# Performance work log

Measured on AMD Instinct MI355X. Metric: run time of the kernel, lower is better.

Reference implementation:

```python
import jax, jax.numpy as jnp
import numpy as np

N = 16384          # nodes
E_R = 524288       # radial edges (avg degree 32)
E_B = 32768        # bonded edges
N_TYPES = 20       # atom types
CS = 64            # scalar (0e) channels
CV = 32            # vector (1o) channels
EA = 16            # edge_attr_dim
EA_B = EA // 2     # bondedness embedding dim
EA_R = (EA + 1) // 2  # radial basis dim
CUTOFF = 1.5       # effective_radial_cutoff
L = 2              # n_layers
NORM = float(np.sqrt((E_R + E_B) / N))  # ~sqrt(avg degree) message normalization


def setup_inputs() -> dict:
    key = jax.random.key(0)
    ks = jax.random.split(key, 32)
    def rn(i, shape, scale=1.0):
        return jax.random.normal(ks[i], shape, dtype=jnp.float32) * scale
    s_e = 1.0 / np.sqrt(EA)
    inp = {}
    inp["pos"] = rn(0, (N, 3))
    inp["c_noise"] = rn(1, (1,))
    inp["atom_types"] = jax.random.randint(ks[2], (N,), 0, N_TYPES)
    inp["radial_edge_index"] = jax.random.randint(ks[3], (2, E_R), 0, N)
    inp["bonded_edge_index"] = jax.random.randint(ks[4], (2, E_B), 0, N)
    # learned parameters
    inp["atom_tab"] = rn(5, (N_TYPES, CS))
    inp["bond_tab"] = rn(6, (2, EA_B))
    inp["ns0_w"] = rn(7, (CS,), 0.1)
    inp["We0"] = rn(8, (EA, CS), s_e)
    inp["We1"] = rn(9, (EA, CS), s_e)
    inp["Wself0"] = rn(10, (CS, CS), 1.0 / np.sqrt(CS))
    inp["Ws0"] = rn(11, (CS, CS), 1.0 / np.sqrt(CS))
    inp["Wv0"] = rn(12, (CS, CV), 1.0 / np.sqrt(CS))
    inp["ns_w"] = rn(13, (L, CS + CV), 0.1)
    inp["We_ss"] = rn(14, (L, EA, CS), s_e)
    inp["We_vs"] = rn(15, (L, EA, CV), s_e)
    inp["We_sv"] = rn(16, (L, EA, CS), s_e)
    inp["We_vv"] = rn(17, (L, EA, CV), s_e)
    inp["We_vx"] = rn(18, (L, EA, CV), s_e)
    inp["Wmix_s"] = rn(19, (L, CS + CV, CS), 1.0 / np.sqrt(CS + CV))
    inp["Wmix_v"] = rn(20, (L, CS + 2 * CV, CV), 1.0 / np.sqrt(CS + 2 * CV))
    inp["Wself_s"] = rn(21, (L, CS, CS), 1.0 / np.sqrt(CS))
    inp["Wself_v"] = rn(22, (L, CV, CV), 1.0 / np.sqrt(CV))
    inp["skip_w"] = rn(23, (L, 2 * (CS + CV)), 0.1)
    inp["skip_b"] = rn(24, (L, 2 * (CS + CV)), 0.1)
    inp["w_out"] = rn(25, (CV,), 1.0 / np.sqrt(CV))
    inp["gain"] = jnp.asarray(0.5, dtype=jnp.float32)
    return inp


def _radial_basis(d):
    # e3nn soft_one_hot_linspace, basis='gaussian', cutoff=True
    centers = jnp.linspace(0.0, CUTOFF, EA_R + 2)[1:-1]
    step = centers[1] - centers[0]
    diff = (d[:, None] - centers[None, :]) / step
    return jnp.exp(-diff * diff) * 1.12


def reference(pos, c_noise, atom_tab, bond_tab, ns0_w, We0, We1, Wself0, Ws0, Wv0,
              ns_w, We_ss, We_vs, We_sv, We_vv, We_vx, Wmix_s, Wmix_v, Wself_s, Wself_v,
              skip_w, skip_b, w_out, gain, atom_types, radial_edge_index, bonded_edge_index):
    edge_index = jnp.concatenate([radial_edge_index, bonded_edge_index], axis=1)
    bond_mask = jnp.concatenate([jnp.zeros((E_R,), jnp.int32), jnp.ones((E_B,), jnp.int32)])
    src, dst = edge_index[0], edge_index[1]
    edge_vec = pos[src] - pos[dst]                      # [E,3]
    d = jnp.sqrt(jnp.sum(edge_vec * edge_vec, -1) + 1e-12)
    Y1 = jnp.sqrt(3.0) * edge_vec / d[:, None]          # l=1 SH, component norm; Y0 == 1
    edge_attr = jnp.concatenate([bond_tab[bond_mask], _radial_basis(d)], axis=-1)  # [E,EA]

    # atom embedding + initial noise-conditional scaling
    s = atom_tab[atom_types] * (1.0 + c_noise * ns0_w)  # [N,CS]

    # initial projector: scalar-input equivariant conv -> hidden irreps
    w0 = edge_attr @ We0
    w1 = edge_attr @ We1
    s_src = s[src]
    a_s = jax.ops.segment_sum(w0 * s_src, dst, num_segments=N) / NORM
    a_v = jax.ops.segment_sum((w1 * s_src)[:, :, None] * Y1[:, None, :], dst, num_segments=N) / NORM
    s_h = a_s @ Ws0 + s @ Wself0                        # [N,CS]
    v_h = jnp.einsum('nci,cd->ndi', a_v, Wv0)           # [N,CV,3]

    for l in range(L):
        # noise-conditional scaling (per-irrep-channel scalar scale)
        scale = 1.0 + c_noise * ns_w[l]
        ss = s_h * scale[:CS]
        vv = v_h * scale[CS:][None, :, None]
        ss_e = ss[src]
        vv_e = vv[src]
        # edge-attr-conditioned tensor-product weights
        w_ss = edge_attr @ We_ss[l]
        w_vs = edge_attr @ We_vs[l]
        w_sv = edge_attr @ We_sv[l]
        w_vv = edge_attr @ We_vv[l]
        w_vx = edge_attr @ We_vx[l]
        # CG tensor-product messages: 0x0->0, 1x1->0 (dot), 0x1->1, 1x0->1, 1x1->1 (cross)
        vdot = jnp.einsum('eci,ei->ec', vv_e, Y1)
        m_s = jnp.concatenate([w_ss * ss_e, w_vs * vdot], axis=-1)          # [E,CS+CV]
        m_v = jnp.concatenate([
            (w_sv * ss_e)[:, :, None] * Y1[:, None, :],
            w_vv[:, :, None] * vv_e,
            w_vx[:, :, None] * jnp.cross(vv_e, Y1[:, None, :]),
        ], axis=1)                                                          # [E,CS+2CV,3]
        a_s = jax.ops.segment_sum(m_s, dst, num_segments=N) / NORM
        a_v = jax.ops.segment_sum(m_v, dst, num_segments=N) / NORM
        new_s = a_s @ Wmix_s[l] + ss @ Wself_s[l]
        new_v = jnp.einsum('nci,cd->ndi', a_v, Wmix_v[l]) + jnp.einsum('nci,cd->ndi', vv, Wself_v[l])
        # noise-conditional skip connection (gated residual)
        g = jax.nn.sigmoid(skip_b[l] + c_noise * skip_w[l])
        s_h = g[:CS] * s_h + g[CS:2 * CS] * new_s
        g_v = g[2 * CS:]
        v_h = g_v[:CV][None, :, None] * v_h + g_v[CV:][None, :, None] * new_v

    # output head: 1o vectors -> 3D displacement, times output gain
    return jnp.einsum('nci,c->ni', v_h, w_out) * gain
```

## Files before the change

### kernel.cpp

```cpp
#include <hip/hip_runtime.h>
#include <math.h>

#define NA 16384
#define ER 524288
#define EB 32768
#define ET 557056
#define INV_NORM 0.17149858514250882f
#define SQRT3 1.7320508075688772f
#define RB_STEP (1.5f/9.0f)
#define BINS 512
#define DMAX 2.5f
#define INV_H ((float)BINS / DMAX)
#define TBLU (2 * BINS * 128)

typedef unsigned int uint32;
typedef unsigned short ushort16;

__device__ __forceinline__ float sigmoidf_(float x) { return 1.f / (1.f + __expf(-x)); }

__device__ __forceinline__ ushort16 f2bf(float x) {
  uint32 u = __float_as_uint(x);
  u = u + 0x7FFFu + ((u >> 16) & 1u);
  return (ushort16)(u >> 16);
}
__device__ __forceinline__ uint32 packbf(float hi, float lo) {
  return ((uint32)f2bf(hi) << 16) | (uint32)f2bf(lo);
}
__device__ __forceinline__ float bfhi(uint32 u) { return __uint_as_float(u & 0xFFFF0000u); }
__device__ __forceinline__ float bflo(uint32 u) { return __uint_as_float(u << 16); }

__device__ __forceinline__ int edge_dst(int e, const int* __restrict__ rad, const int* __restrict__ bon) {
  return (e < ER) ? rad[ER + e] : bon[EB + (e - ER)];
}

__global__ void k_zero(int* __restrict__ count) {
  count[blockIdx.x * 256 + threadIdx.x] = 0;
}

__global__ void k_hist(const int* __restrict__ rad, const int* __restrict__ bon, int* __restrict__ count) {
  int e = blockIdx.x * 256 + threadIdx.x;
  atomicAdd(&count[edge_dst(e, rad, bon)], 1);
}

__global__ void k_scan1(const int* __restrict__ count, int* __restrict__ partial) {
  __shared__ int red[256];
  int b = blockIdx.x, t = threadIdx.x;
  red[t] = count[b * 256 + t];
  __syncthreads();
  for (int s = 128; s > 0; s >>= 1) {
    if (t < s) red[t] += red[t + s];
    __syncthreads();
  }
  if (t == 0) partial[b] = red[0];
}

__global__ void k_scan2(int* __restrict__ partial) {
  int run = 0;
  for (int i = 0; i < 64; ++i) { int c = partial[i]; partial[i] = run; run += c; }
}

__global__ void k_scan3(const int* __restrict__ count, const int* __restrict__ partial,
                        int* __restrict__ offsets, int* __restrict__ cursor) {
  __shared__ int sc[256];
  int b = blockIdx.x, t = threadIdx.x;
  int v = count[b * 256 + t];
  sc[t] = v;
  __syncthreads();
  for (int off = 1; off < 256; off <<= 1) {
    int x = (t >= off) ? sc[t - off] : 0;
    __syncthreads();
    sc[t] += x;
    __syncthreads();
  }
  int excl = sc[t] - v + partial[b];
  offsets[b * 256 + t] = excl;
  cursor[b * 256 + t] = excl;
  if (b == 63 && t == 255) offsets[NA] = excl + v;
}

__global__ void k_fill(const int* __restrict__ rad, const int* __restrict__ bon,
                       int* __restrict__ cursor, int* __restrict__ sorted) {
  int e = blockIdx.x * 256 + threadIdx.x;
  int d = edge_dst(e, rad, bon);
  int slot = atomicAdd(&cursor[d], 1);
  sorted[slot] = e;
}

__global__ void k_edge_pre(const float* __restrict__ pos,
                           const int* __restrict__ rad, const int* __restrict__ bon,
                           const int* __restrict__ sorted, float* __restrict__ rec8) {
  int idx = blockIdx.x * 256 + threadIdx.x;
  int e = sorted[idx];
  int src, dst, v;
  if (e < ER) { src = rad[e]; dst = rad[ER + e]; v = 0; }
  else        { src = bon[e - ER]; dst = bon[EB + e - ER]; v = 1; }
  float dx = pos[src * 3] - pos[dst * 3];
  float dy = pos[src * 3 + 1] - pos[dst * 3 + 1];
  float dz = pos[src * 3 + 2] - pos[dst * 3 + 2];
  float dist = sqrtf(dx * dx + dy * dy + dz * dz + 1e-12f);
  float inv = 1.f / dist;
  float fq = fminf(dist * INV_H, BINS - 1.001f);
  int q = (int)fq;
  float frac = fq - (float)q;
  int qoff = (v * BINS + q) << 7;
  float* rp = rec8 + (size_t)idx * 8;
  *(float4*)rp = make_float4(__int_as_float(src), SQRT3 * dx * inv, SQRT3 * dy * inv, SQRT3 * dz * inv);
  rp[4] = frac;
  rp[5] = __int_as_float(qoff);
}

__global__ void k_build(const float* __restrict__ We0, const float* __restrict__ We1,
                        const float* __restrict__ We_ss, const float* __restrict__ We_vs,
                        const float* __restrict__ We_sv, const float* __restrict__ We_vv,
                        const float* __restrict__ We_vx, const float* __restrict__ bond_tab,
                        uint32* __restrict__ tabs) {
  int q = blockIdx.x, t = blockIdx.y, v = blockIdx.z, c = threadIdx.x;
  float d0 = q * (DMAX / BINS), d1 = (q + 1) * (DMAX / BINS);
  float rb0[8], rb1[8];
#pragma unroll
  for (int k = 0; k < 8; ++k) {
    float f0 = (d0 - (k + 1) * RB_STEP) * (1.f / RB_STEP);
    float f1 = (d1 - (k + 1) * RB_STEP) * (1.f / RB_STEP);
    rb0[k] = 1.12f * __expf(-f0 * f0);
    rb1[k] = 1.12f * __expf(-f1 * f1);
  }
  const float* A;
  const float* B;
  int stride, coff;
  bool hasB = true;
  if (t == 0) { A = We0; B = We1; stride = 64; coff = c; }
  else if (t == 1 || t == 3) {
    int l = (t == 3);
    A = We_ss + l * 1024; B = We_sv + l * 1024; stride = 64; coff = c;
  } else {
    int l = (t == 4);
    stride = 32; coff = c & 31;
    if (c < 32) { A = We_vs + l * 512; B = We_vv + l * 512; }
    else        { A = We_vx + l * 512; B = nullptr; hasB = false; }
  }
  float ba = 0, bb = 0, a0 = 0, a1 = 0, b0 = 0, b1 = 0;
#pragma unroll
  for (int k = 0; k < 8; ++k) {
    float bt = bond_tab[v * 8 + k];
    float av_lo = A[k * stride + coff], av_hi = A[(8 + k) * stride + coff];
    ba += bt * av_lo;
    a0 += rb0[k] * av_hi; a1 += rb1[k] * av_hi;
    if (hasB) {
      float bv_lo = B[k * stride + coff], bv_hi = B[(8 + k) * stride + coff];
      bb += bt * bv_lo;
      b0 += rb0[k] * bv_hi; b1 += rb1[k] * bv_hi;
    }
  }
  uint32* o = tabs + (size_t)t * TBLU + (((size_t)v * BINS + q) << 7) + c * 2;
  o[0] = packbf(ba + a0, a1 - a0);
  o[1] = hasB ? packbf(bb + b0, b1 - b0) : 0u;
}

__global__ void k_embed(const float* __restrict__ atom_tab, const int* __restrict__ types,
                        const float* __restrict__ ns0_w, const float* __restrict__ cnoise,
                        float* __restrict__ s_feat, ushort16* __restrict__ s_bf) {
  int tid = blockIdx.x * 256 + threadIdx.x;
  int n = tid >> 6, c = tid & 63;
  float cn = cnoise[0];
  float v = atom_tab[types[n] * 64 + c] * (1.f + cn * ns0_w[c]);
  s_feat[tid] = v;
  s_bf[tid] = f2bf(v);
}

__global__ __launch_bounds__(256, 6) void k_agg0(
    const int* __restrict__ offsets, const float* __restrict__ rec8,
    const uint32* __restrict__ T0, const ushort16* __restrict__ s_bf,
    float* __restrict__ a_s, float* __restrict__ a_v) {
  int lane = threadIdx.x & 63;
  int n = blockIdx.x * 4 + (threadIdx.x >> 6);
  float acc = 0, a0 = 0, a1 = 0, a2 = 0;
  int beg = __builtin_amdgcn_readfirstlane(offsets[n]);
  int end = __builtin_amdgcn_readfirstlane(offsets[n + 1]);
  if (beg < end) {
    const float* rp0 = rec8 + (size_t)beg * 8;
    float4 rA = *(const float4*)rp0;
    float2 rB = *(const float2*)(rp0 + 4);
    int i1 = beg + (beg + 1 < end ? 1 : 0);
    const float* rp1 = rec8 + (size_t)i1 * 8;
    float4 nA = *(const float4*)rp1;
    float2 nB = *(const float2*)(rp1 + 4);
    uint2 t2 = *(const uint2*)(T0 + __float_as_int(rB.y) + (lane << 1));
    ushort16 su = s_bf[((size_t)__float_as_int(rA.x) << 6) + lane];
#pragma unroll 2
    for (int idx = beg; idx < end; ++idx) {
      uint2 pt2 = *(const uint2*)(T0 + __float_as_int(nB.y) + (lane << 1));
      ushort16 psu = s_bf[((size_t)__float_as_int(nA.x) << 6) + lane];
      int i2 = (idx + 2 < end) ? idx + 2 : end - 1;
      const float* rp2 = rec8 + (size_t)i2 * 8;
      float4 fA = *(const float4*)rp2;
      float2 fB = *(const float2*)(rp2 + 4);
      float frac = rB.x;
      float w0 = fmaf(frac, bflo(t2.x), bfhi(t2.x));
      float w1 = fmaf(frac, bflo(t2.y), bfhi(t2.y));
      float sv = __uint_as_float((uint32)su << 16);
      acc += w0 * sv;
      float t = w1 * sv;
      a0 += t * rA.y; a1 += t * rA.z; a2 += t * rA.w;
      rA = nA; rB = nB; nA = fA; nB = fB; t2 = pt2; su = psu;
    }
  }
  a_s[n * 64 + lane] = acc * INV_NORM;
  *(float4*)(a_v + ((size_t)n << 8) + (lane << 2)) =
      make_float4(a0 * INV_NORM, a1 * INV_NORM, a2 * INV_NORM, 0.f);
}

__global__ __launch_bounds__(256, 6) void k_agg_layer(
    const float* __restrict__ cnoise, const float* __restrict__ nsw,
    const int* __restrict__ offsets, const float* __restrict__ rec8,
    const uint32* __restrict__ TS, const uint32* __restrict__ TU,
    const ushort16* __restrict__ sh_bf, const uint32* __restrict__ vh_bf,
    float* __restrict__ a_s, float* __restrict__ a_v) {
  int lane = threadIdx.x & 63;
  int n = blockIdx.x * 4 + (threadIdx.x >> 6);
  int vc = lane & 31;
  bool low = lane < 32;
  float cn = cnoise[0];
  float scale_s = 1.f + cn * nsw[lane];
  float scale_v = 1.f + cn * nsw[64 + vc];

  float ms = 0;
  float av0 = 0, av1 = 0, av2 = 0;
  float ms2 = 0;
  float b0 = 0, b1 = 0, b2 = 0;
  int beg = __builtin_amdgcn_readfirstlane(offsets[n]);
  int end = __builtin_amdgcn_readfirstlane(offsets[n + 1]);
  if (beg < end) {
    const float* rp0 = rec8 + (size_t)beg * 8;
    float4 rA = *(const float4*)rp0;
    float2 rB = *(const float2*)(rp0 + 4);
    int i1 = beg + (beg + 1 < end ? 1 : 0);
    const float* rp1 = rec8 + (size_t)i1 * 8;
    float4 nA = *(const float4*)rp1;
    float2 nB = *(const float2*)(rp1 + 4);
    int src0 = __float_as_int(rA.x);
    int qo0 = __float_as_int(rB.y);
    uint2 tS = *(const uint2*)(TS + qo0 + (lane << 1));
    uint2 tU = *(const uint2*)(TU + qo0 + (lane << 1));
    ushort16 su = sh_bf[((size_t)src0 << 6) + lane];
    uint2 vv = *(const uint2*)(vh_bf + ((size_t)src0 << 6) + (vc << 1));
#pragma unroll 2
    for (int idx = beg; idx < end; ++idx) {
      int nsrc = __float_as_int(nA.x);
      int nqo = __float_as_int(nB.y);
      uint2 ptS = *(const uint2*)(TS + nqo + (lane << 1));
      uint2 ptU = *(const uint2*)(TU + nqo + (lane << 1));
      ushort16 psu = sh_bf[((size_t)nsrc << 6) + lane];
      uint2 pvv = *(const uint2*)(vh_bf + ((size_t)nsrc << 6) + (vc << 1));
      int i2 = (idx + 2 < end) ? idx + 2 : end - 1;
      const float* rp2 = rec8 + (size_t)i2 * 8;
      float4 fA = *(const float4*)rp2;
      float2 fB = *(const float2*)(rp2 + 4);
      float frac = rB.x;
      float y0 = rA.y, y1 = rA.z, y2 = rA.w;
      float wS  = fmaf(frac, bflo(tS.x), bfhi(tS.x));
      float wSV = fmaf(frac, bflo(tS.y), bfhi(tS.y));
      float wA  = fmaf(frac, bflo(tU.x), bfhi(tU.x));
      float wB  = fmaf(frac, bflo(tU.y), bfhi(tU.y));
      float ss = __uint_as_float((uint32)su << 16);
      float v0 = bfhi(vv.x), v1 = bflo(vv.x), v2 = bfhi(vv.y);
      ms += wS * ss;
      float t = wSV * ss;
      av0 += t * y0; av1 += t * y1; av2 += t * y2;
      float vdot = v0 * y0 + v1 * y1 + v2 * y2;
      ms2 += wA * vdot;
      float cx = v1 * y2 - v2 * y1;
      float cy = v2 * y0 - v0 * y2;
      float cz = v0 * y1 - v1 * y0;
      float m0 = low ? v0 : cx;
      float m1 = low ? v1 : cy;
      float m2 = low ? v2 : cz;
      float wM = low ? wB : wA;
      b0 += wM * m0; b1 += wM * m1; b2 += wM * m2;
      rA = nA; rB = nB; nA = fA; nB = fB;
      tS = ptS; tU = ptU; su = psu; vv = pvv;
    }
  }
  float fs = scale_s * INV_NORM;
  float fv = scale_v * INV_NORM;
  a_s[n * 96 + lane] = ms * fs;
  float* avn = a_v + ((size_t)n << 9);
  *(float4*)(avn + (lane << 2)) = make_float4(av0 * fs, av1 * fs, av2 * fs, 0.f);
  if (low) {
    a_s[n * 96 + 64 + vc] = ms2 * fv;
    *(float4*)(avn + ((64 + vc) << 2)) = make_float4(b0 * fv, b1 * fv, b2 * fv, 0.f);
  } else {
    *(float4*)(avn + ((96 + vc) << 2)) = make_float4(b0 * fv, b1 * fv, b2 * fv, 0.f);
  }
}

__global__ __launch_bounds__(256, 4) void k_init_s(
    const float* __restrict__ a_s, const float* __restrict__ s_feat,
    const float* __restrict__ Ws0, const float* __restrict__ Wself0,
    float* __restrict__ sh, ushort16* __restrict__ sh_bf) {
  __shared__ float W1[64 * 64];
  __shared__ float W2[64 * 64];
  __shared__ float La[8 * 64];
  __shared__ float Lf[8 * 64];
  int tid = threadIdx.x;
  for (int i = tid; i < 1024; i += 256) {
    ((float4*)W1)[i] = ((const float4*)Ws0)[i];
    ((float4*)W2)[i] = ((const float4*)Wself0)[i];
  }
  int base = blockIdx.x * 8;
  for (int i = tid; i < 512; i += 256) {
    La[i] = a_s[(size_t)base * 64 + i];
    Lf[i] = s_feat[(size_t)base * 64 + i];
  }
  __syncthreads();
  int d = tid & 63, g = tid >> 6;
  int n0 = base + g * 2;
  const float* A0 = La + g * 128;
  const float* A1 = A0 + 64;
  const float* F0 = Lf + g * 128;
  const float* F1 = F0 + 64;
  float a0 = 0, a1 = 0;
#pragma unroll 8
  for (int c = 0; c < 64; ++c) {
    float w1 = W1[c * 64 + d], w2 = W2[c * 64 + d];
    a0 += A0[c] * w1 + F0[c] * w2;
    a1 += A1[c] * w1 + F1[c] * w2;
  }
  sh[(size_t)n0 * 64 + d] = a0;
  sh[(size_t)(n0 + 1) * 64 + d] = a1;
  sh_bf[(size_t)n0 * 64 + d] = f2bf(a0);
  sh_bf[(size_t)(n0 + 1) * 64 + d] = f2bf(a1);
}

__global__ __launch_bounds__(256, 4) void k_init_v(
    const float* __restrict__ a_v, const float* __restrict__ Wv0,
    float* __restrict__ vh, uint32* __restrict__ vh_bf) {
  __shared__ float W[64 * 32];
  int tid = threadIdx.x;
  for (int i = tid; i < 512; i += 256) ((float4*)W)[i] = ((const float4*)Wv0)[i];
  __syncthreads();
  int d = tid & 31, g = tid >> 5;
  int n = blockIdx.x * 8 + g;
  const float4* av = (const float4*)(a_v + ((size_t)n << 8));
  float x = 0, y = 0, z = 0;
#pragma unroll 4
  for (int c = 0; c < 64; ++c) {
    float4 a = av[c];
    float w = W[c * 32 + d];
    x += a.x * w; y += a.y * w; z += a.z * w;
  }
  *(float4*)(vh + ((size_t)n << 7) + (d << 2)) = make_float4(x, y, z, 0.f);
  *(uint2*)(vh_bf + ((size_t)n << 6) + (d << 1)) = make_uint2(packbf(x, y), packbf(z, 0.f));
}

__global__ __launch_bounds__(256, 4) void k_mix_s(
    const float* __restrict__ a_s, const float* __restrict__ sh_in,
    const float* __restrict__ Wmix_s, const float* __restrict__ Wself_s,
    const float* __restrict__ nsw, const float* __restrict__ skw,
    const float* __restrict__ skb, const float* __restrict__ cnoise,
    float* __restrict__ sh_out, ushort16* __restrict__ sh_bf_out) {
  __shared__ float Wm[96 * 64];
  __shared__ float Wsf[64 * 64];
  __shared__ float La[8 * 96];
  int tid = threadIdx.x;
  float cn = cnoise[0];
  for (int i = tid; i < 96 * 16; i += 256) ((float4*)Wm)[i] = ((const float4*)Wmix_s)[i];
  for (int i = tid; i < 64 * 16; i += 256) {
    float4 wv = ((const float4*)Wself_s)[i];
    int c = i >> 4;
    float sc = 1.f + cn * nsw[c];
    wv.x *= sc; wv.y *= sc; wv.z *= sc; wv.w *= sc;
    ((float4*)Wsf)[i] = wv;
  }
  int base = blockIdx.x * 8;
  for (int i = tid; i < 8 * 96; i += 256) La[i] = a_s[(size_t)base * 96 + i];
  __syncthreads();
  int d = tid & 63, g = tid >> 6;
  int n0 = base + g * 2;
  const float* A0 = La + (g * 2) * 96;
  const float* A1 = A0 + 96;
  const float* s0p = sh_in + (size_t)n0 * 64;
  const float* s1p = s0p + 64;
  float acc0 = 0, acc1 = 0;
#pragma unroll 8
  for (int c = 0; c < 96; ++c) {
    float w = Wm[c * 64 + d];
    acc0 += A0[c] * w;
    acc1 += A1[c] * w;
  }
#pragma unroll 8
  for (int c = 0; c < 64; ++c) {
    float w = Wsf[c * 64 + d];
    acc0 += s0p[c] * w;
    acc1 += s1p[c] * w;
  }
  float g1 = sigmoidf_(skb[d] + cn * skw[d]);
  float g2 = sigmoidf_(skb[64 + d] + cn * skw[64 + d]);
  float o0 = g1 * s0p[d] + g2 * acc0;
  float o1 = g1 * s1p[d] + g2 * acc1;
  sh_out[(size_t)n0 * 64 + d] = o0;
  sh_out[(size_t)(n0 + 1) * 64 + d] = o1;
  sh_bf_out[(size_t)n0 * 64 + d] = f2bf(o0);
  sh_bf_out[(size_t)(n0 + 1) * 64 + d] = f2bf(o1);
}

__global__ __launch_bounds__(256, 4) void k_mix_v(
    const float* __restrict__ a_v, const float* __restrict__ vh_in,
    const float* __restrict__ Wmix_v, const float* __restrict__ Wself_v,
    const float* __restrict__ nsw, const float* __restrict__ skw,
    const float* __restrict__ skb, const float* __restrict__ cnoise,
    float* __restrict__ vh_out, uint32* __restrict__ vh_bf_out) {
  __shared__ float Wm[128 * 32];
  __shared__ float Wsf[32 * 32];
  int tid = threadIdx.x;
  float cn = cnoise[0];
  for (int i = tid; i < 128 * 8; i += 256) ((float4*)Wm)[i] = ((const float4*)Wmix_v)[i];
  for (int i = tid; i < 32 * 8; i += 256) {
    float4 wv = ((const float4*)Wself_v)[i];
    int c = i >> 3;
    float sc = 1.f + cn * nsw[64 + c];
    wv.x *= sc; wv.y *= sc; wv.z *= sc; wv.w *= sc;
    ((float4*)Wsf)[i] = wv;
  }
  __syncthreads();
  int d = tid & 31, g = tid >> 5;
  int n = blockIdx.x * 8 + g;
  const float4* av = (const float4*)(a_v + ((size_t)n << 9));
  const float4* vr = (const float4*)(vh_in + ((size_t)n << 7));
  float x = 0, y = 0, z = 0;
#pragma unroll 4
  for (int c = 0; c < 128; ++c) {
    float4 a = av[c];
    float w = Wm[c * 32 + d];
    x += a.x * w; y += a.y * w; z += a.z * w;
  }
#pragma unroll 4
  for (int c = 0; c < 32; ++c) {
    float4 vv = vr[c];
    float w = Wsf[c * 32 + d];
    x += vv.x * w; y += vv.y * w; z += vv.z * w;
  }
  float g3 = sigmoidf_(skb[128 + d] + cn * skw[128 + d]);
  float g4 = sigmoidf_(skb[160 + d] + cn * skw[160 + d]);
  float4 vi = vr[d];
  float ox = g3 * vi.x + g4 * x;
  float oy = g3 * vi.y + g4 * y;
  float oz = g3 * vi.z + g4 * z;
  *(float4*)(vh_out + ((size_t)n << 7) + (d << 2)) = make_float4(ox, oy, oz, 0.f);
  *(uint2*)(vh_bf_out + ((size_t)n << 6) + (d << 1)) = make_uint2(packbf(ox, oy), packbf(oz, 0.f));
}

__global__ void k_out(const float* __restrict__ vh, const float* __restrict__ w_out,
                      const float* __restrict__ gain, float* __restrict__ out) {
  int tid = blockIdx.x * 256 + threadIdx.x;
  int n = tid / 3, i = tid - n * 3;
  float acc = 0;
  for (int c = 0; c < 32; ++c) acc += vh[((size_t)n << 7) + c * 4 + i] * w_out[c];
  out[tid] = acc * gain[0];
}

extern "C" void kernel_launch(void* const* d_in, const int* in_sizes, int n_in,
                              void* d_out, int out_size, void* d_ws, size_t ws_size,
                              hipStream_t stream) {
  (void)in_sizes; (void)n_in; (void)out_size; (void)ws_size;
  const float* pos     = (const float*)d_in[0];
  const float* cn      = (const float*)d_in[1];
  const int*   types   = (const int*)d_in[2];
  const int*   rad     = (const int*)d_in[3];
  const int*   bon     = (const int*)d_in[4];
  const float* atom_tab= (const float*)d_in[5];
  const float* bond_tab= (const float*)d_in[6];
  const float* ns0_w   = (const float*)d_in[7];
  const float* We0     = (const float*)d_in[8];
  const float* We1     = (const float*)d_in[9];
  const float* Wself0  = (const float*)d_in[10];
  const float* Ws0     = (const float*)d_in[11];
  const float* Wv0     = (const float*)d_in[12];
  const float* ns_w    = (const float*)d_in[13];
  const float* We_ss   = (const float*)d_in[14];
  const float* We_vs   = (const float*)d_in[15];
  const float* We_sv   = (const float*)d_in[16];
  const float* We_vv   = (const float*)d_in[17];
  const float* We_vx   = (const float*)d_in[18];
  const float* Wmix_s  = (const float*)d_in[19];
  const float* Wmix_v  = (const float*)d_in[20];
  const float* Wself_s = (const float*)d_in[21];
  const float* Wself_v = (const float*)d_in[22];
  const float* skip_w  = (const float*)d_in[23];
  const float* skip_b  = (const float*)d_in[24];
  const float* w_out   = (const float*)d_in[25];
  const float* gain    = (const float*)d_in[26];

  char* ws = (char*)d_ws;
  size_t o = 0;
  auto alloc = [&](size_t bytes) -> void* {
    void* p = ws + o;
    o += (bytes + 255) & ~(size_t)255;
    return p;
  };
  float* s_feat  = (float*)alloc((size_t)NA * 64 * 4);
  ushort16* s_bf = (ushort16*)alloc((size_t)NA * 64 * 2);
  float* a_s     = (float*)alloc((size_t)NA * 96 * 4);
  float* a_v     = (float*)alloc((size_t)NA * 512 * 4);
  float* sh0     = (float*)alloc((size_t)NA * 64 * 4);
  float* sh1     = (float*)alloc((size_t)NA * 64 * 4);
  ushort16* shbf0= (ushort16*)alloc((size_t)NA * 64 * 2);
  ushort16* shbf1= (ushort16*)alloc((size_t)NA * 64 * 2);
  float* vh0     = (float*)alloc((size_t)NA * 128 * 4);
  float* vh1     = (float*)alloc((size_t)NA * 128 * 4);
  uint32* vhbf0  = (uint32*)alloc((size_t)NA * 64 * 4);
  uint32* vhbf1  = (uint32*)alloc((size_t)NA * 64 * 4);
  int* count     = (int*)alloc((size_t)NA * 4);
  int* partial   = (int*)alloc((size_t)64 * 4);
  int* offsets   = (int*)alloc((size_t)(NA + 1) * 4);
  int* cursor    = (int*)alloc((size_t)NA * 4);
  int* sorted    = (int*)alloc((size_t)ET * 4);
  float* rec8    = (float*)alloc((size_t)ET * 32);
  uint32* tabs   = (uint32*)alloc((size_t)5 * TBLU * 4);
  float* shb[2]  = {sh0, sh1};
  ushort16* shbf[2] = {shbf0, shbf1};
  float* vhb[2]  = {vh0, vh1};
  uint32* vhbf[2]= {vhbf0, vhbf1};

  k_zero<<<NA / 256, 256, 0, stream>>>(count);
  k_hist<<<ET / 256, 256, 0, stream>>>(rad, bon, count);
  k_scan1<<<64, 256, 0, stream>>>(count, partial);
  k_scan2<<<1, 1, 0, stream>>>(partial);
  k_scan3<<<64, 256, 0, stream>>>(count, partial, offsets, cursor);
  k_fill<<<ET / 256, 256, 0, stream>>>(rad, bon, cursor, sorted);
  k_edge_pre<<<ET / 256, 256, 0, stream>>>(pos, rad, bon, sorted, rec8);
  k_build<<<dim3(BINS, 5, 2), 64, 0, stream>>>(We0, We1, We_ss, We_vs, We_sv, We_vv, We_vx,
                                               bond_tab, tabs);

  k_embed<<<NA * 64 / 256, 256, 0, stream>>>(atom_tab, types, ns0_w, cn, s_feat, s_bf);
  k_agg0<<<NA / 4, 256, 0, stream>>>(offsets, rec8, tabs, s_bf, a_s, a_v);
  k_init_s<<<NA / 8, 256, 0, stream>>>(a_s, s_feat, Ws0, Wself0, shb[0], shbf[0]);
  k_init_v<<<NA / 8, 256, 0, stream>>>(a_v, Wv0, vhb[0], vhbf[0]);

  for (int l = 0; l < 2; ++l) {
    int bin = l & 1, bout = 1 - bin;
    const uint32* TS = tabs + (size_t)(1 + 2 * l) * TBLU;
    const uint32* TU = tabs + (size_t)(2 + 2 * l) * TBLU;
    k_agg_layer<<<NA / 4, 256, 0, stream>>>(
        cn, ns_w + l * 96, offsets, rec8, TS, TU, shbf[bin], vhbf[bin], a_s, a_v);
    k_mix_s<<<NA / 8, 256, 0, stream>>>(
        a_s, shb[bin], Wmix_s + l * 96 * 64, Wself_s + l * 64 * 64,
        ns_w + l * 96, skip_w + l * 192, skip_b + l * 192, cn, shb[bout], shbf[bout]);
    k_mix_v<<<NA / 8, 256, 0, stream>>>(
        a_v, vhb[bin], Wmix_v + l * 128 * 32, Wself_v + l * 32 * 32,
        ns_w + l * 96, skip_w + l * 192, skip_b + l * 192, cn, vhb[bout], vhbf[bout]);
  }
  k_out<<<NA * 3 / 256, 256, 0, stream>>>(vhb[0], w_out, gain, (float*)d_out);
}
```

Baseline: 526.8 us.

## Fuse edge fill with preprocessing, interleave layer weight tables, deepen aggregation prefetch

Merges the counting-sort fill and the edge preprocessing into one kernel. Each edge now writes its record straight to its atomically assigned slot, so the sorted index array and its extra pass go away. The per-layer scalar and vector weight tables become one interleaved table, so each lane fetches a single 16-byte uint4 per edge instead of two 8-byte loads. The aggregation kernels move from a two-deep to a three-deep software prefetch pipeline and raise the launch-bounds occupancy hint from 6 to 8. The cost is higher register pressure and a slightly different edge order within each node segment.

```diff
diff --git a/kernel.cpp b/kernel.cpp
--- a/kernel.cpp
+++ b/kernel.cpp
@@ -11,7 +11,8 @@
 #define BINS 512
 #define DMAX 2.5f
 #define INV_H ((float)BINS / DMAX)
-#define TBLU (2 * BINS * 128)
+#define T0U (2 * BINS * 128)
+#define TLU (2 * BINS * 256)
 
 typedef unsigned int uint32;
 typedef unsigned short ushort16;
@@ -29,17 +30,14 @@
 __device__ __forceinline__ float bfhi(uint32 u) { return __uint_as_float(u & 0xFFFF0000u); }
 __device__ __forceinline__ float bflo(uint32 u) { return __uint_as_float(u << 16); }
 
-__device__ __forceinline__ int edge_dst(int e, const int* __restrict__ rad, const int* __restrict__ bon) {
-  return (e < ER) ? rad[ER + e] : bon[EB + (e - ER)];
-}
-
 __global__ void k_zero(int* __restrict__ count) {
   count[blockIdx.x * 256 + threadIdx.x] = 0;
 }
 
 __global__ void k_hist(const int* __restrict__ rad, const int* __restrict__ bon, int* __restrict__ count) {
   int e = blockIdx.x * 256 + threadIdx.x;
-  atomicAdd(&count[edge_dst(e, rad, bon)], 1);
+  int d = (e < ER) ? rad[ER + e] : bon[EB + (e - ER)];
+  atomicAdd(&count[d], 1);
 }
 
 __global__ void k_scan1(const int* __restrict__ count, int* __restrict__ partial) {
@@ -78,19 +76,10 @@
   if (b == 63 && t == 255) offsets[NA] = excl + v;
 }
 
-__global__ void k_fill(const int* __restrict__ rad, const int* __restrict__ bon,
-                       int* __restrict__ cursor, int* __restrict__ sorted) {
+__global__ void k_fill_pre(const int* __restrict__ rad, const int* __restrict__ bon,
+                           int* __restrict__ cursor, const float* __restrict__ pos,
+                           float* __restrict__ rec8) {
   int e = blockIdx.x * 256 + threadIdx.x;
-  int d = edge_dst(e, rad, bon);
-  int slot = atomicAdd(&cursor[d], 1);
-  sorted[slot] = e;
-}
-
-__global__ void k_edge_pre(const float* __restrict__ pos,
-                           const int* __restrict__ rad, const int* __restrict__ bon,
-                           const int* __restrict__ sorted, float* __restrict__ rec8) {
-  int idx = blockIdx.x * 256 + threadIdx.x;
-  int e = sorted[idx];
   int src, dst, v;
   if (e < ER) { src = rad[e]; dst = rad[ER + e]; v = 0; }
   else        { src = bon[e - ER]; dst = bon[EB + e - ER]; v = 1; }
@@ -102,18 +91,19 @@
   float fq = fminf(dist * INV_H, BINS - 1.001f);
   int q = (int)fq;
   float frac = fq - (float)q;
-  int qoff = (v * BINS + q) << 7;
-  float* rp = rec8 + (size_t)idx * 8;
+  int qoffL = (v * BINS + q) << 8;
+  int slot = atomicAdd(&cursor[dst], 1);
+  float* rp = rec8 + (size_t)slot * 8;
   *(float4*)rp = make_float4(__int_as_float(src), SQRT3 * dx * inv, SQRT3 * dy * inv, SQRT3 * dz * inv);
   rp[4] = frac;
-  rp[5] = __int_as_float(qoff);
+  rp[5] = __int_as_float(qoffL);
 }
 
 __global__ void k_build(const float* __restrict__ We0, const float* __restrict__ We1,
                         const float* __restrict__ We_ss, const float* __restrict__ We_vs,
                         const float* __restrict__ We_sv, const float* __restrict__ We_vv,
                         const float* __restrict__ We_vx, const float* __restrict__ bond_tab,
-                        uint32* __restrict__ tabs) {
+                        uint32* __restrict__ T0, uint32* __restrict__ TL) {
   int q = blockIdx.x, t = blockIdx.y, v = blockIdx.z, c = threadIdx.x;
   float d0 = q * (DMAX / BINS), d1 = (q + 1) * (DMAX / BINS);
   float rb0[8], rb1[8];
@@ -124,36 +114,52 @@
     rb0[k] = 1.12f * __expf(-f0 * f0);
     rb1[k] = 1.12f * __expf(-f1 * f1);
   }
-  const float* A;
-  const float* B;
-  int stride, coff;
-  bool hasB = true;
-  if (t == 0) { A = We0; B = We1; stride = 64; coff = c; }
-  else if (t == 1 || t == 3) {
-    int l = (t == 3);
-    A = We_ss + l * 1024; B = We_sv + l * 1024; stride = 64; coff = c;
-  } else {
-    int l = (t == 4);
-    stride = 32; coff = c & 31;
-    if (c < 32) { A = We_vs + l * 512; B = We_vv + l * 512; }
-    else        { A = We_vx + l * 512; B = nullptr; hasB = false; }
-  }
-  float ba = 0, bb = 0, a0 = 0, a1 = 0, b0 = 0, b1 = 0;
+  if (t == 0) {
+    float ba = 0, bb = 0, a0 = 0, a1 = 0, b0 = 0, b1 = 0;
 #pragma unroll
-  for (int k = 0; k < 8; ++k) {
-    float bt = bond_tab[v * 8 + k];
-    float av_lo = A[k * stride + coff], av_hi = A[(8 + k) * stride + coff];
-    ba += bt * av_lo;
-    a0 += rb0[k] * av_hi; a1 += rb1[k] * av_hi;
-    if (hasB) {
-      float bv_lo = B[k * stride + coff], bv_hi = B[(8 + k) * stride + coff];
-      bb += bt * bv_lo;
+    for (int k = 0; k < 8; ++k) {
+      float bt = bond_tab[v * 8 + k];
+      float av_lo = We0[k * 64 + c], av_hi = We0[(8 + k) * 64 + c];
+      float bv_lo = We1[k * 64 + c], bv_hi = We1[(8 + k) * 64 + c];
+      ba += bt * av_lo; bb += bt * bv_lo;
+      a0 += rb0[k] * av_hi; a1 += rb1[k] * av_hi;
       b0 += rb0[k] * bv_hi; b1 += rb1[k] * bv_hi;
     }
-  }
-  uint32* o = tabs + (size_t)t * TBLU + (((size_t)v * BINS + q) << 7) + c * 2;
-  o[0] = packbf(ba + a0, a1 - a0);
-  o[1] = hasB ? packbf(bb + b0, b1 - b0) : 0u;
+    uint32* o = T0 + (((size_t)v * BINS + q) << 7) + c * 2;
+    o[0] = packbf(ba + a0, a1 - a0);
+    o[1] = packbf(bb + b0, b1 - b0);
+  } else {
+    int l = t - 1;
+    const float* Wss = We_ss + l * 1024;
+    const float* Wsv = We_sv + l * 1024;
+    const float* WA = (c < 32) ? (We_vs + l * 512) : (We_vx + l * 512);
+    const float* WB = (c < 32) ? (We_vv + l * 512) : nullptr;
+    int cu = c & 31;
+    float sa = 0, sb = 0, s0 = 0, s1 = 0, t0 = 0, t1 = 0;
+    float ua = 0, ub = 0, u0 = 0, u1 = 0, w0 = 0, w1 = 0;
+#pragma unroll
+    for (int k = 0; k < 8; ++k) {
+      float bt = bond_tab[v * 8 + k];
+      float ss_lo = Wss[k * 64 + c], ss_hi = Wss[(8 + k) * 64 + c];
+      float sv_lo = Wsv[k * 64 + c], sv_hi = Wsv[(8 + k) * 64 + c];
+      sa += bt * ss_lo; sb += bt * sv_lo;
+      s0 += rb0[k] * ss_hi; s1 += rb1[k] * ss_hi;
+      t0 += rb0[k] * sv_hi; t1 += rb1[k] * sv_hi;
+      float a_lo = WA[k * 32 + cu], a_hi = WA[(8 + k) * 32 + cu];
+      ua += bt * a_lo;
+      u0 += rb0[k] * a_hi; u1 += rb1[k] * a_hi;
+      if (WB) {
+        float b_lo = WB[k * 32 + cu], b_hi = WB[(8 + k) * 32 + cu];
+        ub += bt * b_lo;
+        w0 += rb0[k] * b_hi; w1 += rb1[k] * b_hi;
+      }
+    }
+    uint32* o = TL + (size_t)l * TLU + (((size_t)v * BINS + q) << 8) + c * 4;
+    o[0] = packbf(sa + s0, s1 - s0);
+    o[1] = packbf(sb + t0, t1 - t0);
+    o[2] = packbf(ua + u0, u1 - u0);
+    o[3] = WB ? packbf(ub + w0, w1 - w0) : 0u;
+  }
 }
 
 __global__ void k_embed(const float* __restrict__ atom_tab, const int* __restrict__ types,
@@ -167,7 +173,7 @@
   s_bf[tid] = f2bf(v);
 }
 
-__global__ __launch_bounds__(256, 6) void k_agg0(
+__global__ __launch_bounds__(256, 8) void k_agg0(
     const int* __restrict__ offsets, const float* __restrict__ rec8,
     const uint32* __restrict__ T0, const ushort16* __restrict__ s_bf,
     float* __restrict__ a_s, float* __restrict__ a_v) {
@@ -177,31 +183,35 @@
   int beg = __builtin_amdgcn_readfirstlane(offsets[n]);
   int end = __builtin_amdgcn_readfirstlane(offsets[n + 1]);
   if (beg < end) {
-    const float* rp0 = rec8 + (size_t)beg * 8;
-    float4 rA = *(const float4*)rp0;
-    float2 rB = *(const float2*)(rp0 + 4);
-    int i1 = beg + (beg + 1 < end ? 1 : 0);
-    const float* rp1 = rec8 + (size_t)i1 * 8;
-    float4 nA = *(const float4*)rp1;
-    float2 nB = *(const float2*)(rp1 + 4);
-    uint2 t2 = *(const uint2*)(T0 + __float_as_int(rB.y) + (lane << 1));
-    ushort16 su = s_bf[((size_t)__float_as_int(rA.x) << 6) + lane];
-#pragma unroll 2
+    int last = end - 1;
+    int e1 = (beg + 1 < end) ? beg + 1 : last;
+    int e2 = (beg + 2 < end) ? beg + 2 : last;
+    const float* p0 = rec8 + (size_t)beg * 8;
+    const float* p1 = rec8 + (size_t)e1 * 8;
+    const float* p2 = rec8 + (size_t)e2 * 8;
+    float4 rA0 = *(const float4*)p0; float2 rB0 = *(const float2*)(p0 + 4);
+    float4 rA1 = *(const float4*)p1; float2 rB1 = *(const float2*)(p1 + 4);
+    float4 rA2 = *(const float4*)p2; float2 rB2 = *(const float2*)(p2 + 4);
+    uint2 t0 = *(const uint2*)(T0 + (__float_as_int(rB0.y) >> 1) + (lane << 1));
+    ushort16 s0 = s_bf[((size_t)__float_as_int(rA0.x) << 6) + lane];
+    uint2 t1 = *(const uint2*)(T0 + (__float_as_int(rB1.y) >> 1) + (lane << 1));
+    ushort16 s1 = s_bf[((size_t)__float_as_int(rA1.x) << 6) + lane];
+#pragma unroll 3
     for (int idx = beg; idx < end; ++idx) {
-      uint2 pt2 = *(const uint2*)(T0 + __float_as_int(nB.y) + (lane << 1));
-      ushort16 psu = s_bf[((size_t)__float_as_int(nA.x) << 6) + lane];
-      int i2 = (idx + 2 < end) ? idx + 2 : end - 1;
-      const float* rp2 = rec8 + (size_t)i2 * 8;
-      float4 fA = *(const float4*)rp2;
-      float2 fB = *(const float2*)(rp2 + 4);
-      float frac = rB.x;
-      float w0 = fmaf(frac, bflo(t2.x), bfhi(t2.x));
-      float w1 = fmaf(frac, bflo(t2.y), bfhi(t2.y));
-      float sv = __uint_as_float((uint32)su << 16);
+      uint2 t2 = *(const uint2*)(T0 + (__float_as_int(rB2.y) >> 1) + (lane << 1));
+      ushort16 s2 = s_bf[((size_t)__float_as_int(rA2.x) << 6) + lane];
+      int e3 = (idx + 3 < end) ? idx + 3 : last;
+      const float* p3 = rec8 + (size_t)e3 * 8;
+      float4 rA3 = *(const float4*)p3; float2 rB3 = *(const float2*)(p3 + 4);
+      float frac = rB0.x;
+      float w0 = fmaf(frac, bflo(t0.x), bfhi(t0.x));
+      float w1 = fmaf(frac, bflo(t0.y), bfhi(t0.y));
+      float sv = __uint_as_float((uint32)s0 << 16);
       acc += w0 * sv;
       float t = w1 * sv;
-      a0 += t * rA.y; a1 += t * rA.z; a2 += t * rA.w;
-      rA = nA; rB = nB; nA = fA; nB = fB; t2 = pt2; su = psu;
+      a0 += t * rA0.y; a1 += t * rA0.z; a2 += t * rA0.w;
+      rA0 = rA1; rB0 = rB1; rA1 = rA2; rB1 = rB2; rA2 = rA3; rB2 = rB3;
+      t0 = t1; s0 = s1; t1 = t2; s1 = s2;
     }
   }
   a_s[n * 64 + lane] = acc * INV_NORM;
@@ -209,11 +219,11 @@
       make_float4(a0 * INV_NORM, a1 * INV_NORM, a2 * INV_NORM, 0.f);
 }
 
-__global__ __launch_bounds__(256, 6) void k_agg_layer(
+__global__ __launch_bounds__(256, 8) void k_agg_layer(
     const float* __restrict__ cnoise, const float* __restrict__ nsw,
     const int* __restrict__ offsets, const float* __restrict__ rec8,
-    const uint32* __restrict__ TS, const uint32* __restrict__ TU,
-    const ushort16* __restrict__ sh_bf, const uint32* __restrict__ vh_bf,
+    const uint32* __restrict__ TL, const ushort16* __restrict__ sh_bf,
+    const uint32* __restrict__ vh_bf,
     float* __restrict__ a_s, float* __restrict__ a_v) {
   int lane = threadIdx.x & 63;
   int n = blockIdx.x * 4 + (threadIdx.x >> 6);
@@ -230,54 +240,52 @@
   int beg = __builtin_amdgcn_readfirstlane(offsets[n]);
   int end = __builtin_amdgcn_readfirstlane(offsets[n + 1]);
   if (beg < end) {
-    const float* rp0 = rec8 + (size_t)beg * 8;
-    float4 rA = *(const float4*)rp0;
-    float2 rB = *(const float2*)(rp0 + 4);
-    int i1 = beg + (beg + 1 < end ? 1 : 0);
-    const float* rp1 = rec8 + (size_t)i1 * 8;
-    float4 nA = *(const float4*)rp1;
-    float2 nB = *(const float2*)(rp1 + 4);
-    int src0 = __float_as_int(rA.x);
-    int qo0 = __float_as_int(rB.y);
-    uint2 tS = *(const uint2*)(TS + qo0 + (lane << 1));
-    uint2 tU = *(const uint2*)(TU + qo0 + (lane << 1));
-    ushort16 su = sh_bf[((size_t)src0 << 6) + lane];
-    uint2 vv = *(const uint2*)(vh_bf + ((size_t)src0 << 6) + (vc << 1));
-#pragma unroll 2
+    int last = end - 1;
+    int e1 = (beg + 1 < end) ? beg + 1 : last;
+    int e2 = (beg + 2 < end) ? beg + 2 : last;
+    const float* p0 = rec8 + (size_t)beg * 8;
+    const float* p1 = rec8 + (size_t)e1 * 8;
+    const float* p2 = rec8 + (size_t)e2 * 8;
+    float4 rA0 = *(const float4*)p0; float2 rB0 = *(const float2*)(p0 + 4);
+    float4 rA1 = *(const float4*)p1; float2 rB1 = *(const float2*)(p1 + 4);
+    float4 rA2 = *(const float4*)p2; float2 rB2 = *(const float2*)(p2 + 4);
+    uint4 t0 = *(const uint4*)(TL + __float_as_int(rB0.y) + (lane << 2));
+    ushort16 s0 = sh_bf[((size_t)__float_as_int(rA0.x) << 6) + lane];
+    uint2 v0 = *(const uint2*)(vh_bf + ((size_t)__float_as_int(rA0.x) << 6) + (vc << 1));
+    uint4 t1 = *(const uint4*)(TL + __float_as_int(rB1.y) + (lane << 2));
+    ushort16 s1 = sh_bf[((size_t)__float_as_int(rA1.x) << 6) + lane];
+    uint2 v1 = *(const uint2*)(vh_bf + ((size_t)__float_as_int(rA1.x) << 6) + (vc << 1));
+#pragma unroll 3
     for (int idx = beg; idx < end; ++idx) {
-      int nsrc = __float_as_int(nA.x);
-      int nqo = __float_as_int(nB.y);
-      uint2 ptS = *(const uint2*)(TS + nqo + (lane << 1));
-      uint2 ptU = *(const uint2*)(TU + nqo + (lane << 1));
-      ushort16 psu = sh_bf[((size_t)nsrc << 6) + lane];
-      uint2 pvv = *(const uint2*)(vh_bf + ((size_t)nsrc << 6) + (vc << 1));
-      int i2 = (idx + 2 < end) ? idx + 2 : end - 1;
-      const float* rp2 = rec8 + (size_t)i2 * 8;
-      float4 fA = *(const float4*)rp2;
-      float2 fB = *(const float2*)(rp2 + 4);
-      float frac = rB.x;
-      float y0 = rA.y, y1 = rA.z, y2 = rA.w;
-      float wS  = fmaf(frac, bflo(tS.x), bfhi(tS.x));
-      float wSV = fmaf(frac, bflo(tS.y), bfhi(tS.y));
-      float wA  = fmaf(frac, bflo(tU.x), bfhi(tU.x));
-      float wB  = fmaf(frac, bflo(tU.y), bfhi(tU.y));
-      float ss = __uint_as_float((uint32)su << 16);
-      float v0 = bfhi(vv.x), v1 = bflo(vv.x), v2 = bfhi(vv.y);
+      uint4 t2 = *(const uint4*)(TL + __float_as_int(rB2.y) + (lane << 2));
+      ushort16 s2 = sh_bf[((size_t)__float_as_int(rA2.x) << 6) + lane];
+      uint2 v2 = *(const uint2*)(vh_bf + ((size_t)__float_as_int(rA2.x) << 6) + (vc << 1));
+      int e3 = (idx + 3 < end) ? idx + 3 : last;
+      const float* p3 = rec8 + (size_t)e3 * 8;
+      float4 rA3 = *(const float4*)p3; float2 rB3 = *(const float2*)(p3 + 4);
+      float frac = rB0.x;
+      float y0 = rA0.y, y1 = rA0.z, y2 = rA0.w;
+      float wS  = fmaf(frac, bflo(t0.x), bfhi(t0.x));
+      float wSV = fmaf(frac, bflo(t0.y), bfhi(t0.y));
+      float wA  = fmaf(frac, bflo(t0.z), bfhi(t0.z));
+      float wB  = fmaf(frac, bflo(t0.w), bfhi(t0.w));
+      float ss = __uint_as_float((uint32)s0 << 16);
+      float vx = bfhi(v0.x), vy = bflo(v0.x), vz = bfhi(v0.y);
       ms += wS * ss;
       float t = wSV * ss;
       av0 += t * y0; av1 += t * y1; av2 += t * y2;
-      float vdot = v0 * y0 + v1 * y1 + v2 * y2;
+      float vdot = vx * y0 + vy * y1 + vz * y2;
       ms2 += wA * vdot;
-      float cx = v1 * y2 - v2 * y1;
-      float cy = v2 * y0 - v0 * y2;
-      float cz = v0 * y1 - v1 * y0;
-      float m0 = low ? v0 : cx;
-      float m1 = low ? v1 : cy;
-      float m2 = low ? v2 : cz;
+      float cx = vy * y2 - vz * y1;
+      float cy = vz * y0 - vx * y2;
+      float cz = vx * y1 - vy * y0;
+      float m0 = low ? vx : cx;
+      float m1 = low ? vy : cy;
+      float m2 = low ? vz : cz;
       float wM = low ? wB : wA;
       b0 += wM * m0; b1 += wM * m1; b2 += wM * m2;
-      rA = nA; rB = nB; nA = fA; nB = fB;
-      tS = ptS; tU = ptU; su = psu; vv = pvv;
+      rA0 = rA1; rB0 = rB1; rA1 = rA2; rB1 = rB2; rA2 = rA3; rB2 = rB3;
+      t0 = t1; s0 = s1; v0 = v1; t1 = t2; s1 = s2; v1 = v2;
     }
   }
   float fs = scale_s * INV_NORM;
@@ -513,9 +521,9 @@
   int* partial   = (int*)alloc((size_t)64 * 4);
   int* offsets   = (int*)alloc((size_t)(NA + 1) * 4);
   int* cursor    = (int*)alloc((size_t)NA * 4);
-  int* sorted    = (int*)alloc((size_t)ET * 4);
   float* rec8    = (float*)alloc((size_t)ET * 32);
-  uint32* tabs   = (uint32*)alloc((size_t)5 * TBLU * 4);
+  uint32* T0     = (uint32*)alloc((size_t)T0U * 4);
+  uint32* TL     = (uint32*)alloc((size_t)2 * TLU * 4);
   float* shb[2]  = {sh0, sh1};
   ushort16* shbf[2] = {shbf0, shbf1};
   float* vhb[2]  = {vh0, vh1};
@@ -526,22 +534,19 @@
   k_scan1<<<64, 256, 0, stream>>>(count, partial);
   k_scan2<<<1, 1, 0, stream>>>(partial);
   k_scan3<<<64, 256, 0, stream>>>(count, partial, offsets, cursor);
-  k_fill<<<ET / 256, 256, 0, stream>>>(rad, bon, cursor, sorted);
-  k_edge_pre<<<ET / 256, 256, 0, stream>>>(pos, rad, bon, sorted, rec8);
-  k_build<<<dim3(BINS, 5, 2), 64, 0, stream>>>(We0, We1, We_ss, We_vs, We_sv, We_vv, We_vx,
-                                               bond_tab, tabs);
+  k_fill_pre<<<ET / 256, 256, 0, stream>>>(rad, bon, cursor, pos, rec8);
+  k_build<<<dim3(BINS, 3, 2), 64, 0, stream>>>(We0, We1, We_ss, We_vs, We_sv, We_vv, We_vx,
+                                               bond_tab, T0, TL);
 
   k_embed<<<NA * 64 / 256, 256, 0, stream>>>(atom_tab, types, ns0_w, cn, s_feat, s_bf);
-  k_agg0<<<NA / 4, 256, 0, stream>>>(offsets, rec8, tabs, s_bf, a_s, a_v);
+  k_agg0<<<NA / 4, 256, 0, stream>>>(offsets, rec8, T0, s_bf, a_s, a_v);
   k_init_s<<<NA / 8, 256, 0, stream>>>(a_s, s_feat, Ws0, Wself0, shb[0], shbf[0]);
   k_init_v<<<NA / 8, 256, 0, stream>>>(a_v, Wv0, vhb[0], vhbf[0]);
 
   for (int l = 0; l < 2; ++l) {
     int bin = l & 1, bout = 1 - bin;
-    const uint32* TS = tabs + (size_t)(1 + 2 * l) * TBLU;
-    const uint32* TU = tabs + (size_t)(2 + 2 * l) * TBLU;
     k_agg_layer<<<NA / 4, 256, 0, stream>>>(
-        cn, ns_w + l * 96, offsets, rec8, TS, TU, shbf[bin], vhbf[bin], a_s, a_v);
+        cn, ns_w + l * 96, offsets, rec8, TL + (size_t)l * TLU, shbf[bin], vhbf[bin], a_s, a_v);
     k_mix_s<<<NA / 8, 256, 0, stream>>>(
         a_s, shb[bin], Wmix_s + l * 96 * 64, Wself_s + l * 64 * 64,
         ns_w + l * 96, skip_w + l * 192, skip_b + l * 192, cn, shb[bout], shbf[bout]);
```

Result: faster. 470.7 us (-10.7%).
